# Kernel optimization log

Measured on AMD Instinct MI355X. Metric: run time of the kernel, lower is better.

## Reference

```python
import jax, jax.numpy as jnp
import numpy as np

B, N, S, CIN, COUT, GDIM = 4, 128, 8, 8, 8, 7  # batch, points, coset samples, channels, g_embed+2*q_embed


def setup_inputs() -> dict:
    key = jax.random.key(0)
    ks = jax.random.split(key, 8)
    pairwise_g = jax.random.normal(ks[0], (B, N, N, S, S, GDIM), jnp.float32)
    coset_functions = jax.random.normal(ks[1], (B, N, S, CIN), jnp.float32)
    mask = jax.random.bernoulli(ks[2], 0.9, (B, N, S))  # bool key mask (B,N,S)
    # per-channel SumKernel params: k_y = Linear(2->1), k_g = Linear(GDIM->1), stacked over CIN channels
    w_y = jax.random.normal(ks[3], (CIN, 2), jnp.float32) * 0.1
    b_y = jax.random.normal(ks[4], (CIN,), jnp.float32) * 0.1
    w_g = jax.random.normal(ks[5], (CIN, GDIM), jnp.float32) * 0.1
    b_g = jax.random.normal(ks[6], (CIN,), jnp.float32) * 0.1
    w_lin = jax.random.normal(ks[7], (COUT, CIN), jnp.float32) * (1.0 / np.sqrt(CIN))
    return {"pairwise_g": pairwise_g, "coset_functions": coset_functions, "mask": mask,
            "w_y": w_y, "b_y": b_y, "w_g": w_g, "b_g": b_g, "w_lin": w_lin}


def reference(pairwise_g, coset_functions, mask, w_y, b_y, w_g, b_g, w_lin):
    # Vectorized over the original per-channel Python loop: channel axis c.
    y = coset_functions  # (B, N, S, C)
    # k_g(pairwise_g) per channel + both biases: (B,i,j,s1,s2,C)
    logits = jnp.einsum('bijstg,cg->bijstc', pairwise_g, w_g) + (b_g + b_y)
    # k_y([y_1, y_2]): y_1 indexed by key (j, s2) -> weight w_y[:,0]; y_2 by query (i, s1) -> w_y[:,1]
    key_term = y * w_y[:, 0]   # (B, N, S, C)
    qry_term = y * w_y[:, 1]   # (B, N, S, C)
    logits = logits + key_term[:, None, :, None, :, :] + qry_term[:, :, None, :, None, :]
    # plain exp (original does NOT subtract a max), zero out masked keys (j, s2)
    att = jnp.where(mask[:, None, :, None, :, None], jnp.exp(logits), 0.0)
    att = att / att.sum(axis=(2, 4), keepdims=True)  # normalize over key dims
    # weighted sum of key values over (j, s2), residual add
    out = y + jnp.einsum('bijstc,bjtc->bisc', att, y)
    out = out * mask[..., None].astype(out.dtype)
    # output linear c_in -> c_out, no bias (torch Linear: x @ W.T)
    return out @ w_lin.T
```

## Files before the change

kernel.cpp:

```cpp
#include <hip/hip_runtime.h>


namespace {

constexpr int kB = 4, kN = 128, kS = 8, kC = 8, kO = 8, kG = 7;
constexpr int JSTRIDE = 68;

__global__ __launch_bounds__(256, 2)
void emha_kernel(const float* __restrict__ pg,
                 const float* __restrict__ y,
                 const int*   __restrict__ mask,
                 const float* __restrict__ w_y,
                 const float* __restrict__ w_g,
                 const float* __restrict__ w_lin,
                 float*       __restrict__ out)
{
    __shared__ float lds_kw[kN * JSTRIDE];
    __shared__ float lds_kv[kN * JSTRIDE];
    __shared__ float red[4][8][16];
    __shared__ float obuf[8][8];

    const int t  = threadIdx.x;
    const int bi = blockIdx.x;
    const int b  = bi >> 7;
    const int i  = bi & 127;

    float wg[kC][kG];
#pragma unroll
    for (int c = 0; c < kC; ++c)
#pragma unroll
        for (int g = 0; g < kG; ++g)
            wg[c][g] = w_g[c * kG + g];

    const float* yb = y    + b * (kN * kS * kC);
    const int*   mb = mask + b * (kN * kS);
    const float  wy0 = w_y[2 * (t & 7)];
#pragma unroll
    for (int k = 0; k < 32; ++k) {
        const int idx = t + k * 256;
        const float yv = yb[idx];
        const int   m  = mb[idx >> 3];
        const float kw = m ? __expf(yv * wy0) : 0.0f;
        const int off = (idx >> 6) * JSTRIDE + (idx & 63);
        lds_kw[off] = kw;
        lds_kv[off] = kw * yv;
    }
    __syncthreads();

    const float* pbase = pg + (size_t)bi * (kN * kS * kS * kG);
    const int s1 = t & 7;
    float num[kC], den[kC];
#pragma unroll
    for (int c = 0; c < kC; ++c) { num[c] = 0.0f; den[c] = 0.0f; }

#pragma unroll
    for (int k = 0; k < 4; ++k) {
        const int j    = k * 32 + (t >> 3);
        const int pair = k * 256 + t;
        const float4* src = reinterpret_cast<const float4*>(pbase + (size_t)pair * 56);
        float p[56];
#pragma unroll
        for (int q = 0; q < 14; ++q)
            reinterpret_cast<float4*>(p)[q] = src[q];

#pragma unroll
        for (int s2 = 0; s2 < kS; ++s2) {
            const int lo = j * JSTRIDE + s2 * 8;
            const float4 kva = *reinterpret_cast<const float4*>(&lds_kv[lo]);
            const float4 kvb = *reinterpret_cast<const float4*>(&lds_kv[lo + 4]);
            const float4 kwa = *reinterpret_cast<const float4*>(&lds_kw[lo]);
            const float4 kwb = *reinterpret_cast<const float4*>(&lds_kw[lo + 4]);
            const float kv[8] = {kva.x, kva.y, kva.z, kva.w, kvb.x, kvb.y, kvb.z, kvb.w};
            const float kw[8] = {kwa.x, kwa.y, kwa.z, kwa.w, kwb.x, kwb.y, kwb.z, kwb.w};
#pragma unroll
            for (int c = 0; c < kC; ++c) {
                float d =      p[s2 * kG + 0] * wg[c][0];
                d = fmaf(p[s2 * kG + 1], wg[c][1], d);
                d = fmaf(p[s2 * kG + 2], wg[c][2], d);
                d = fmaf(p[s2 * kG + 3], wg[c][3], d);
                d = fmaf(p[s2 * kG + 4], wg[c][4], d);
                d = fmaf(p[s2 * kG + 5], wg[c][5], d);
                d = fmaf(p[s2 * kG + 6], wg[c][6], d);
                const float e = __expf(d);
                num[c] = fmaf(e, kv[c], num[c]);
                den[c] = fmaf(e, kw[c], den[c]);
            }
        }
    }

#pragma unroll
    for (int c = 0; c < kC; ++c) {
        num[c] += __shfl_xor(num[c], 8);
        num[c] += __shfl_xor(num[c], 16);
        num[c] += __shfl_xor(num[c], 32);
        den[c] += __shfl_xor(den[c], 8);
        den[c] += __shfl_xor(den[c], 16);
        den[c] += __shfl_xor(den[c], 32);
    }
    const int wave = t >> 6;
    const int lane = t & 63;
    if (lane < 8) {
#pragma unroll
        for (int c = 0; c < kC; ++c) {
            red[wave][lane][c]     = num[c];
            red[wave][lane][c + 8] = den[c];
        }
    }
    __syncthreads();

    if (t < 64) {
        const int s1q = t >> 3, c = t & 7;
        float ns = 0.0f, ds = 0.0f;
#pragma unroll
        for (int w = 0; w < 4; ++w) { ns += red[w][s1q][c]; ds += red[w][s1q][c + 8]; }
        const float yv = yb[(i * kS + s1q) * kC + c];
        const int   m  = mb[i * kS + s1q];
        obuf[s1q][c] = m ? (yv + ns / ds) : 0.0f;
    }
    __syncthreads();

    if (t < 64) {
        const int s1q = t >> 3, o = t & 7;
        float acc = 0.0f;
#pragma unroll
        for (int c = 0; c < kC; ++c)
            acc = fmaf(obuf[s1q][c], w_lin[o * kC + c], acc);
        out[(size_t)bi * (kS * kO) + t] = acc;
    }
}

}

extern "C" void kernel_launch(void* const* d_in, const int* in_sizes, int n_in,
                              void* d_out, int out_size, void* d_ws, size_t ws_size,
                              hipStream_t stream)
{
    const float* pg    = (const float*)d_in[0];
    const float* y     = (const float*)d_in[1];
    const int*   mask  = (const int*)  d_in[2];
    const float* w_y   = (const float*)d_in[3];
    const float* w_g   = (const float*)d_in[5];
    const float* w_lin = (const float*)d_in[7];
    float* out = (float*)d_out;

    emha_kernel<<<kB * kN, 256, 0, stream>>>(pg, y, mask, w_y, w_g, w_lin, out);
}
```

Before: 27.71 us.

## Split key dimension across four blocks and add finalize reduction kernel

The single kernel with one block per (b,i) query is split into a partial kernel that gives each block a quarter of the keys (32 j's) and writes partial numerator/denominator sums to workspace. A second small kernel combines the four partials, applies the division, residual, mask and output linear. This quadruples the block count (2048 vs 512) and shrinks LDS per block so more blocks can be resident, with pg loads issued up front. The cost is an extra launch and a workspace round trip.

After: 33.27 us. 1.2x slower.

```diff
diff --git a/kernel.cpp b/kernel.cpp
--- a/kernel.cpp
+++ b/kernel.cpp
@@ -3,27 +3,34 @@
 
 namespace {
 
-constexpr int kB = 4, kN = 128, kS = 8, kC = 8, kO = 8, kG = 7;
+constexpr int kN = 128, kS = 8, kC = 8, kO = 8, kG = 7;
+constexpr int kSplit = 4;
+constexpr int kBI = 4 * kN;
 constexpr int JSTRIDE = 68;
 
-__global__ __launch_bounds__(256, 2)
-void emha_kernel(const float* __restrict__ pg,
-                 const float* __restrict__ y,
-                 const int*   __restrict__ mask,
-                 const float* __restrict__ w_y,
-                 const float* __restrict__ w_g,
-                 const float* __restrict__ w_lin,
-                 float*       __restrict__ out)
+__global__ __launch_bounds__(256, 4)
+void emha_partial(const float* __restrict__ pg,
+                  const float* __restrict__ y,
+                  const int*   __restrict__ mask,
+                  const float* __restrict__ w_y,
+                  const float* __restrict__ w_g,
+                  float*       __restrict__ ws)
 {
-    __shared__ float lds_kw[kN * JSTRIDE];
-    __shared__ float lds_kv[kN * JSTRIDE];
+    __shared__ float lds_kw[32 * JSTRIDE];
+    __shared__ float lds_kv[32 * JSTRIDE];
     __shared__ float red[4][8][16];
-    __shared__ float obuf[8][8];
 
-    const int t  = threadIdx.x;
-    const int bi = blockIdx.x;
-    const int b  = bi >> 7;
-    const int i  = bi & 127;
+    const int t     = threadIdx.x;
+    const int blk   = blockIdx.x;
+    const int split = blk & 3;
+    const int bi    = blk >> 2;
+    const int b     = bi >> 7;
+
+    const float4* src = reinterpret_cast<const float4*>(
+        pg + ((size_t)bi * 1024 + 256 * split + t) * 56);
+    float4 pv[14];
+#pragma unroll
+    for (int q = 0; q < 14; ++q) pv[q] = src[q];
 
     float wg[kC][kG];
 #pragma unroll
@@ -32,11 +39,11 @@
         for (int g = 0; g < kG; ++g)
             wg[c][g] = w_g[c * kG + g];
 
-    const float* yb = y    + b * (kN * kS * kC);
-    const int*   mb = mask + b * (kN * kS);
+    const float* yb = y    + b * (kN * kS * kC) + split * 2048;
+    const int*   mb = mask + b * (kN * kS)      + split * 256;
     const float  wy0 = w_y[2 * (t & 7)];
 #pragma unroll
-    for (int k = 0; k < 32; ++k) {
+    for (int k = 0; k < 8; ++k) {
         const int idx = t + k * 256;
         const float yv = yb[idx];
         const int   m  = mb[idx >> 3];
@@ -47,44 +54,33 @@
     }
     __syncthreads();
 
-    const float* pbase = pg + (size_t)bi * (kN * kS * kS * kG);
-    const int s1 = t & 7;
+    const int jl = t >> 3;
+    const float* p = reinterpret_cast<const float*>(pv);
     float num[kC], den[kC];
 #pragma unroll
     for (int c = 0; c < kC; ++c) { num[c] = 0.0f; den[c] = 0.0f; }
 
 #pragma unroll
-    for (int k = 0; k < 4; ++k) {
-        const int j    = k * 32 + (t >> 3);
-        const int pair = k * 256 + t;
-        const float4* src = reinterpret_cast<const float4*>(pbase + (size_t)pair * 56);
-        float p[56];
+    for (int s2 = 0; s2 < kS; ++s2) {
+        const int lo = jl * JSTRIDE + s2 * 8;
+        const float4 kva = *reinterpret_cast<const float4*>(&lds_kv[lo]);
+        const float4 kvb = *reinterpret_cast<const float4*>(&lds_kv[lo + 4]);
+        const float4 kwa = *reinterpret_cast<const float4*>(&lds_kw[lo]);
+        const float4 kwb = *reinterpret_cast<const float4*>(&lds_kw[lo + 4]);
+        const float kv[8] = {kva.x, kva.y, kva.z, kva.w, kvb.x, kvb.y, kvb.z, kvb.w};
+        const float kw[8] = {kwa.x, kwa.y, kwa.z, kwa.w, kwb.x, kwb.y, kwb.z, kwb.w};
 #pragma unroll
-        for (int q = 0; q < 14; ++q)
-            reinterpret_cast<float4*>(p)[q] = src[q];
-
-#pragma unroll
-        for (int s2 = 0; s2 < kS; ++s2) {
-            const int lo = j * JSTRIDE + s2 * 8;
-            const float4 kva = *reinterpret_cast<const float4*>(&lds_kv[lo]);
-            const float4 kvb = *reinterpret_cast<const float4*>(&lds_kv[lo + 4]);
-            const float4 kwa = *reinterpret_cast<const float4*>(&lds_kw[lo]);
-            const float4 kwb = *reinterpret_cast<const float4*>(&lds_kw[lo + 4]);
-            const float kv[8] = {kva.x, kva.y, kva.z, kva.w, kvb.x, kvb.y, kvb.z, kvb.w};
-            const float kw[8] = {kwa.x, kwa.y, kwa.z, kwa.w, kwb.x, kwb.y, kwb.z, kwb.w};
-#pragma unroll
-            for (int c = 0; c < kC; ++c) {
-                float d =      p[s2 * kG + 0] * wg[c][0];
-                d = fmaf(p[s2 * kG + 1], wg[c][1], d);
-                d = fmaf(p[s2 * kG + 2], wg[c][2], d);
-                d = fmaf(p[s2 * kG + 3], wg[c][3], d);
-                d = fmaf(p[s2 * kG + 4], wg[c][4], d);
-                d = fmaf(p[s2 * kG + 5], wg[c][5], d);
-                d = fmaf(p[s2 * kG + 6], wg[c][6], d);
-                const float e = __expf(d);
-                num[c] = fmaf(e, kv[c], num[c]);
-                den[c] = fmaf(e, kw[c], den[c]);
-            }
+        for (int c = 0; c < kC; ++c) {
+            float d =      p[s2 * kG + 0] * wg[c][0];
+            d = fmaf(p[s2 * kG + 1], wg[c][1], d);
+            d = fmaf(p[s2 * kG + 2], wg[c][2], d);
+            d = fmaf(p[s2 * kG + 3], wg[c][3], d);
+            d = fmaf(p[s2 * kG + 4], wg[c][4], d);
+            d = fmaf(p[s2 * kG + 5], wg[c][5], d);
+            d = fmaf(p[s2 * kG + 6], wg[c][6], d);
+            const float e = __expf(d);
+            num[c] = fmaf(e, kv[c], num[c]);
+            den[c] = fmaf(e, kw[c], den[c]);
         }
     }
 
@@ -108,25 +104,58 @@
     }
     __syncthreads();
 
-    if (t < 64) {
-        const int s1q = t >> 3, c = t & 7;
-        float ns = 0.0f, ds = 0.0f;
+    if (t < 128) {
+        float v = 0.0f;
 #pragma unroll
-        for (int w = 0; w < 4; ++w) { ns += red[w][s1q][c]; ds += red[w][s1q][c + 8]; }
-        const float yv = yb[(i * kS + s1q) * kC + c];
-        const int   m  = mb[i * kS + s1q];
-        obuf[s1q][c] = m ? (yv + ns / ds) : 0.0f;
+        for (int w = 0; w < 4; ++w) v += red[w][t >> 4][t & 15];
+        ws[(size_t)(split * kBI + bi) * 128 + t] = v;
     }
-    __syncthreads();
+}
 
-    if (t < 64) {
-        const int s1q = t >> 3, o = t & 7;
+__global__ __launch_bounds__(256)
+void emha_finalize(const float* __restrict__ ws,
+                   const float* __restrict__ y,
+                   const int*   __restrict__ mask,
+                   const float* __restrict__ w_lin,
+                   float*       __restrict__ out)
+{
+    const int tid = blockIdx.x * 256 + threadIdx.x;
+    const int bi  = tid >> 3;
+    const int s1  = tid & 7;
+
+    float4 n0 = {0,0,0,0}, n1 = {0,0,0,0}, d0 = {0,0,0,0}, d1 = {0,0,0,0};
+#pragma unroll
+    for (int s = 0; s < kSplit; ++s) {
+        const float4* pp = reinterpret_cast<const float4*>(
+            ws + (size_t)(s * kBI + bi) * 128 + s1 * 16);
+        const float4 a = pp[0], bq = pp[1], cq = pp[2], dq = pp[3];
+        n0.x += a.x;  n0.y += a.y;  n0.z += a.z;  n0.w += a.w;
+        n1.x += bq.x; n1.y += bq.y; n1.z += bq.z; n1.w += bq.w;
+        d0.x += cq.x; d0.y += cq.y; d0.z += cq.z; d0.w += cq.w;
+        d1.x += dq.x; d1.y += dq.y; d1.z += dq.z; d1.w += dq.w;
+    }
+    const float nn[8] = {n0.x, n0.y, n0.z, n0.w, n1.x, n1.y, n1.z, n1.w};
+    const float dd[8] = {d0.x, d0.y, d0.z, d0.w, d1.x, d1.y, d1.z, d1.w};
+
+    const float* yrow = y + (size_t)bi * 64 + s1 * 8;
+    const int m = mask[bi * 8 + s1];
+    float ob[8];
+#pragma unroll
+    for (int c = 0; c < kC; ++c)
+        ob[c] = m ? (yrow[c] + nn[c] / dd[c]) : 0.0f;
+
+    float o[8];
+#pragma unroll
+    for (int oo = 0; oo < kO; ++oo) {
         float acc = 0.0f;
 #pragma unroll
         for (int c = 0; c < kC; ++c)
-            acc = fmaf(obuf[s1q][c], w_lin[o * kC + c], acc);
-        out[(size_t)bi * (kS * kO) + t] = acc;
+            acc = fmaf(ob[c], w_lin[oo * kC + c], acc);
+        o[oo] = acc;
     }
+    float4* op = reinterpret_cast<float4*>(out + (size_t)bi * 64 + s1 * 8);
+    op[0] = make_float4(o[0], o[1], o[2], o[3]);
+    op[1] = make_float4(o[4], o[5], o[6], o[7]);
 }
 
 }
@@ -142,6 +171,8 @@
     const float* w_g   = (const float*)d_in[5];
     const float* w_lin = (const float*)d_in[7];
     float* out = (float*)d_out;
+    float* wsf = (float*)d_ws;
 
-    emha_kernel<<<kB * kN, 256, 0, stream>>>(pg, y, mask, w_y, w_g, w_lin, out);
+    emha_partial<<<kBI * kSplit, 256, 0, stream>>>(pg, y, mask, w_y, w_g, wsf);
+    emha_finalize<<<16, 256, 0, stream>>>(wsf, y, mask, w_lin, out);
 }
```
